# Kernel optimization log

Measured on AMD Instinct MI355X. Metric: run time of the kernel, lower is better.

Reference implementation:

```python
import jax, jax.numpy as jnp
import numpy as np

NUM_HEADS = 16
EPS = 1e-06


def setup_inputs() -> dict:
    key = jax.random.key(0)
    ks = jax.random.split(key, 6)
    b, s, d = 4, 4096, 1024
    scale = 1.0 / np.sqrt(d)
    return {
        "x": jax.random.normal(ks[0], (b, s, d), dtype=jnp.float32),
        "wq": jax.random.normal(ks[1], (d, d), dtype=jnp.float32) * scale,
        "wk": jax.random.normal(ks[2], (d, d), dtype=jnp.float32) * scale,
        "wv": jax.random.normal(ks[3], (d, d), dtype=jnp.float32) * scale,
        "wo": jax.random.normal(ks[4], (d, d), dtype=jnp.float32) * scale,
        "bo": jnp.zeros((d,), dtype=jnp.float32),
    }


def _split_heads(t, h):
    b, s, d = t.shape
    return t.reshape(b, s, h, d // h).transpose(0, 2, 1, 3)  # [b,h,s,dh]


def reference(x, wq, wk, wv, wo, bo):
    h = NUM_HEADS
    # torch Linear: y = x @ W.T (no bias for q/k/v)
    q = _split_heads(x @ wq.T, h)
    k = _split_heads(x @ wk.T, h)
    v = _split_heads(x @ wv.T, h)
    # ELU+1 feature map
    qf = jax.nn.elu(q) + 1.0
    kf = jax.nn.elu(k) + 1.0
    # global key feature sum over sequence: [b,h,dh]
    k_sum = jnp.sum(kf, axis=-2)
    # denominator: [b,h,s,1]
    denom = jnp.sum(qf * k_sum[:, :, None, :], axis=-1, keepdims=True) + EPS
    # kv = sum_s kf_s (outer) v_s  -> [b,h,dh,dh]  (the broadcast-sum in torch == matmul)
    kv = jnp.einsum('bhsd,bhse->bhde', kf, v)
    # q_kv: [b,h,s,dh]
    q_kv = jnp.einsum('bhsd,bhde->bhse', qf, kv)
    out = q_kv / denom
    b, _, s, dh = out.shape
    out = out.transpose(0, 2, 1, 3).reshape(b, s, h * dh)  # merge heads
    return out @ wo.T + bo
```

## Files before the change

### kernel.cpp

```cpp
#include <hip/hip_runtime.h>
#include <hip/hip_bf16.h>
#include <cmath>


#define TOK    16384
#define DMODEL 1024
#define NHEAD  16
#define DH     64
#define KSPLIT 8

using bf16x8 = __attribute__((ext_vector_type(8))) short;
using f32x4  = __attribute__((ext_vector_type(4))) float;

typedef __attribute__((address_space(1))) const unsigned int gld_src_t;
typedef __attribute__((address_space(3))) unsigned int gld_dst_t;

__device__ __forceinline__ unsigned short f2bf(float x) {
    unsigned int u = __float_as_uint(x);
    u += 0x7fffu + ((u >> 16) & 1u);
    return (unsigned short)(u >> 16);
}
__device__ __forceinline__ float bf2f(unsigned short b) {
    return __uint_as_float((unsigned int)b << 16);
}

__global__ __launch_bounds__(256) void split_k(
    const float* __restrict__ in, unsigned short* __restrict__ hi,
    unsigned short* __restrict__ lo, int n)
{
    int i = (blockIdx.x * 256 + threadIdx.x) * 4;
    if (i >= n) return;
    float4 v = *(const float4*)(in + i);
    float vs[4] = {v.x, v.y, v.z, v.w};
    unsigned short hh[4], ll[4];
#pragma unroll
    for (int j = 0; j < 4; ++j) {
        unsigned short h = f2bf(vs[j]);
        hh[j] = h;
        ll[j] = f2bf(vs[j] - bf2f(h));
    }
    *(ushort4*)(hi + i) = make_ushort4(hh[0], hh[1], hh[2], hh[3]);
    *(ushort4*)(lo + i) = make_ushort4(ll[0], ll[1], ll[2], ll[3]);
}

__global__ __launch_bounds__(256) void splitw_k(
    const float* __restrict__ w0, const float* __restrict__ w1,
    const float* __restrict__ w2, const float* __restrict__ w3,
    unsigned short* __restrict__ hs, unsigned short* __restrict__ ls)
{
    int w = blockIdx.x >> 10;
    const float* src = (w == 0) ? w0 : (w == 1) ? w1 : (w == 2) ? w2 : w3;
    int i = ((blockIdx.x & 1023) * 256 + threadIdx.x) * 4;
    size_t base = (size_t)w * (DMODEL * DMODEL);
    float4 v = *(const float4*)(src + i);
    float vs[4] = {v.x, v.y, v.z, v.w};
    unsigned short hh[4], ll[4];
#pragma unroll
    for (int j = 0; j < 4; ++j) {
        unsigned short h = f2bf(vs[j]);
        hh[j] = h;
        ll[j] = f2bf(vs[j] - bf2f(h));
    }
    *(ushort4*)(hs + base + i) = make_ushort4(hh[0], hh[1], hh[2], hh[3]);
    *(ushort4*)(ls + base + i) = make_ushort4(ll[0], ll[1], ll[2], ll[3]);
}

template<int ACT>
__global__ __launch_bounds__(512, 2) void gemm256_k(
    const unsigned short* __restrict__ Ah, const unsigned short* __restrict__ Al,
    const unsigned short* __restrict__ Bh, const unsigned short* __restrict__ Bl,
    const float* __restrict__ bias, float* __restrict__ C,
    unsigned short* __restrict__ Ch, unsigned short* __restrict__ Cl,
    int M, int N, int K)
{
    __shared__ unsigned short lds[2][4][256 * 32];
    const int tid  = threadIdx.x;
    const int lane = tid & 63, wid = tid >> 6;

    const int nwg = gridDim.x, cpx = nwg >> 3;
    const int g = ((int)blockIdx.x & 7) * cpx + ((int)blockIdx.x >> 3);
    const int m0 = (g >> 2) * 256, n0 = (g & 3) * 256;

    const int wr = wid >> 2, wc = wid & 3;
    const int fr = lane & 15, ko = lane >> 4;

    f32x4 acc[8][4];
#pragma unroll
    for (int i = 0; i < 8; ++i)
#pragma unroll
        for (int j = 0; j < 4; ++j) acc[i][j] = (f32x4){0.f, 0.f, 0.f, 0.f};

    const unsigned short* srcb = (wid < 2) ? Ah : (wid < 4) ? Al : (wid < 6) ? Bh : Bl;
    const int rowbase = ((wid < 4) ? m0 : n0) + (wid & 1) * 128;
    const int rloc = (wid & 1) * 128 + (lane >> 2);
    const int sslot = (lane & 3) ^ ((rloc >> 1) & 3);
    const unsigned short* gsrc0 = srcb + (size_t)(rowbase + (lane >> 2)) * K + sslot * 8;
    const int mat  = wid >> 1;
    const int ldso = ((wid & 1) * 128) * 32;

    const int koff = (ko ^ ((fr >> 1) & 3)) * 8;
    const int abase = (wr * 128 + fr) * 32 + koff;
    const int bbase = (wc * 64 + fr) * 32 + koff;
    const int nt = K / 32;

#pragma unroll
    for (int u = 0; u < 8; ++u) {
        __builtin_amdgcn_global_load_lds((gld_src_t*)(gsrc0 + (size_t)u * 16 * K),
            (gld_dst_t*)&lds[0][mat][ldso + u * 512], 16, 0, 0);
    }
    asm volatile("s_waitcnt vmcnt(0)" ::: "memory");
    __builtin_amdgcn_s_barrier();

    for (int t = 0; t < nt; ++t) {
        const int cur = t & 1;
        const bool hv = (t + 1 < nt);
        const unsigned short* gk = gsrc0 + (size_t)(t + 1) * 32;
        unsigned short* ldsn = &lds[cur ^ 1][mat][ldso];
        bf16x8 Bh_[4], Bl_[4];

#pragma unroll
        for (int p = 0; p < 4; ++p) {
            if (hv) {
#pragma unroll
                for (int q = 0; q < 2; ++q) {
                    int u = p * 2 + q;
                    __builtin_amdgcn_global_load_lds((gld_src_t*)(gk + (size_t)u * 16 * K),
                        (gld_dst_t*)(ldsn + u * 512), 16, 0, 0);
                }
            }
            if (p == 0) {
                if (hv) asm volatile("s_waitcnt vmcnt(2)" ::: "memory");
                else    asm volatile("s_waitcnt vmcnt(0)" ::: "memory");
                __builtin_amdgcn_s_barrier();
            }
            int aoff0 = abase + (2 * p) * 16 * 32;
            bf16x8 ah0 = *(const bf16x8*)&lds[cur][0][aoff0];
            bf16x8 al0 = *(const bf16x8*)&lds[cur][1][aoff0];
            bf16x8 ah1 = *(const bf16x8*)&lds[cur][0][aoff0 + 512];
            bf16x8 al1 = *(const bf16x8*)&lds[cur][1][aoff0 + 512];
            if (p == 0) {
#pragma unroll
                for (int nj = 0; nj < 4; ++nj) {
                    int boff = bbase + nj * 16 * 32;
                    Bh_[nj] = *(const bf16x8*)&lds[cur][2][boff];
                    Bl_[nj] = *(const bf16x8*)&lds[cur][3][boff];
                }
            }
            __builtin_amdgcn_s_barrier();
            asm volatile("s_waitcnt lgkmcnt(0)" ::: "memory");
            __builtin_amdgcn_sched_barrier(0);
            __builtin_amdgcn_s_setprio(1);
#pragma unroll
            for (int nj = 0; nj < 4; ++nj) {
                acc[2*p  ][nj] = __builtin_amdgcn_mfma_f32_16x16x32_bf16(ah0, Bh_[nj], acc[2*p  ][nj], 0, 0, 0);
                acc[2*p  ][nj] = __builtin_amdgcn_mfma_f32_16x16x32_bf16(ah0, Bl_[nj], acc[2*p  ][nj], 0, 0, 0);
                acc[2*p  ][nj] = __builtin_amdgcn_mfma_f32_16x16x32_bf16(al0, Bh_[nj], acc[2*p  ][nj], 0, 0, 0);
                acc[2*p+1][nj] = __builtin_amdgcn_mfma_f32_16x16x32_bf16(ah1, Bh_[nj], acc[2*p+1][nj], 0, 0, 0);
                acc[2*p+1][nj] = __builtin_amdgcn_mfma_f32_16x16x32_bf16(ah1, Bl_[nj], acc[2*p+1][nj], 0, 0, 0);
                acc[2*p+1][nj] = __builtin_amdgcn_mfma_f32_16x16x32_bf16(al1, Bh_[nj], acc[2*p+1][nj], 0, 0, 0);
            }
            __builtin_amdgcn_s_setprio(0);
            __builtin_amdgcn_s_barrier();
        }
    }

    const int fq = ko;
#pragma unroll
    for (int mi = 0; mi < 8; ++mi) {
#pragma unroll
        for (int i = 0; i < 4; ++i) {
            int m = m0 + wr * 128 + mi * 16 + fq * 4 + i;
            size_t rbase = (size_t)m * N + n0 + wc * 64;
#pragma unroll
            for (int nj = 0; nj < 4; ++nj) {
                int n = nj * 16 + fr;
                float v = acc[mi][nj][i];
                if (ACT == 1 || ACT == 3) v = (v > 0.f) ? (v + 1.f) : expf(v);
                if (ACT == 2) v += bias[n0 + wc * 64 + n];
                if (ACT == 3) {
                    unsigned short hb = f2bf(v);
                    Ch[rbase + n] = hb;
                    Cl[rbase + n] = f2bf(v - bf2f(hb));
                } else {
                    C[rbase + n] = v;
                }
            }
        }
    }
}

__global__ __launch_bounds__(256) void kv_partial_k(
    const float* __restrict__ kf, const float* __restrict__ vchunk,
    int bh_base, float* __restrict__ kvp, float* __restrict__ ksp)
{
    __shared__ float kfs[8][64];
    __shared__ float vs[8][64];
    const int bh = bh_base + blockIdx.x;
    const int split = blockIdx.y;
    const int b = bh >> 4, h = bh & 15;
    const int blocal = b - (bh_base >> 4);
    const int tid = threadIdx.x;
    const int col = tid & 63, rg = tid >> 6;
    const int tx = tid & 15, ty = tid >> 4;
    const int di0 = ty * 4, dj0 = tx * 4;

    float acc[4][4] = {};
    float ks[4] = {0.f, 0.f, 0.f, 0.f};

    const int rows = 4096 / KSPLIT;
    const size_t kbase = ((size_t)b * 4096 + (size_t)split * rows) * DMODEL + h * DH;
    const size_t vbase = ((size_t)blocal * 4096 + (size_t)split * rows) * DMODEL + h * DH;

    for (int it = 0; it < rows / 8; ++it) {
        __syncthreads();
#pragma unroll
        for (int p = 0; p < 2; ++p) {
            int r = rg + p * 4;
            size_t o = (size_t)(it * 8 + r) * DMODEL + col;
            kfs[r][col] = kf[kbase + o];
            vs[r][col]  = vchunk[vbase + o];
        }
        __syncthreads();
#pragma unroll
        for (int r = 0; r < 8; ++r) {
            float a[4], bb[4];
#pragma unroll
            for (int i = 0; i < 4; ++i) a[i] = kfs[r][di0 + i];
#pragma unroll
            for (int j = 0; j < 4; ++j) bb[j] = vs[r][dj0 + j];
#pragma unroll
            for (int i = 0; i < 4; ++i)
#pragma unroll
                for (int j = 0; j < 4; ++j)
                    acc[i][j] = fmaf(a[i], bb[j], acc[i][j]);
            if (tx == 0) {
#pragma unroll
                for (int i = 0; i < 4; ++i) ks[i] += a[i];
            }
        }
    }

    const size_t obase = ((size_t)(bh * KSPLIT + split)) * (DH * DH);
#pragma unroll
    for (int i = 0; i < 4; ++i)
#pragma unroll
        for (int j = 0; j < 4; ++j)
            kvp[obase + (size_t)(di0 + i) * DH + dj0 + j] = acc[i][j];
    if (tx == 0) {
        size_t kb = ((size_t)(bh * KSPLIT + split)) * DH + di0;
#pragma unroll
        for (int i = 0; i < 4; ++i) ksp[kb + i] = ks[i];
    }
}

__global__ __launch_bounds__(256) void reduce_kv_k(
    const float* __restrict__ kvp, const float* __restrict__ ksp,
    unsigned short* __restrict__ kvth, unsigned short* __restrict__ kvtl)
{
    int idx = blockIdx.x * 256 + threadIdx.x;
    int bh = idx >> 12, off = idx & 4095;
    int d = off & 63, e = off >> 6;
    float s = 0.f;
    for (int c = 0; c < KSPLIT; ++c) s += kvp[((size_t)(bh * KSPLIT + c)) * 4096 + d * 64 + e];
    unsigned short hb = f2bf(s);
    size_t o = (size_t)bh * (96 * 64) + (size_t)e * 64 + d;
    kvth[o] = hb;
    kvtl[o] = f2bf(s - bf2f(hb));
    if (idx < 64 * DH) {
        int bh2 = idx >> 6, d2 = idx & 63;
        float t = 0.f;
        for (int c = 0; c < KSPLIT; ++c) t += ksp[((size_t)(bh2 * KSPLIT + c)) * DH + d2];
        unsigned short h2 = f2bf(t);
        size_t o2 = (size_t)bh2 * (96 * 64) + 64 * 64 + d2;
        kvth[o2] = h2;
        kvtl[o2] = f2bf(t - bf2f(h2));
    }
}

__global__ __launch_bounds__(512, 2) void attn_mfma_k(
    const unsigned short* __restrict__ qh, const unsigned short* __restrict__ ql,
    const unsigned short* __restrict__ kvth, const unsigned short* __restrict__ kvtl,
    unsigned short* __restrict__ out_hi, unsigned short* __restrict__ out_lo)
{
    __shared__ unsigned short lds[28672];
    __shared__ float denoms[128];
    const int tid = threadIdx.x, lane = tid & 63, wid = tid >> 6;
    const int blk = blockIdx.x;
    const int bh = blk >> 5, tb = blk & 31;
    const int b = bh >> 4, h = bh & 15;
    const int t0 = b * 4096 + tb * 128;

    const int l8 = lane >> 3, s7 = lane & 7;
#pragma unroll
    for (int shot = 0; shot < 7; ++shot) {
        int r = wid * 7 + shot;
        const unsigned short* src;
        int dstE;
        if (r < 32) {
            int row = (r & 15) * 8 + l8;
            int sslot = s7 ^ (row & 7);
            src = ((r < 16) ? qh : ql) + (size_t)(t0 + row) * DMODEL + h * DH + sslot * 8;
            dstE = ((r < 16) ? 0 : 8192) + (r & 15) * 512;
        } else {
            int rb = r - 32;
            int rl = (rb < 12) ? rb : rb - 12;
            int row = rl * 8 + l8;
            int sslot = s7 ^ (row & 7);
            src = ((rb < 12) ? kvth : kvtl) + (size_t)bh * (96 * 64) + row * 64 + sslot * 8;
            dstE = ((rb < 12) ? 16384 : 22528) + rl * 512;
        }
        __builtin_amdgcn_global_load_lds((gld_src_t*)src, (gld_dst_t*)&lds[dstE], 16, 0, 0);
    }
    __syncthreads();

    const int fr = lane & 15, ko = lane >> 4, fq = ko;
    const int arow = wid * 16 + fr;

    f32x4 acc[5];
#pragma unroll
    for (int nj = 0; nj < 5; ++nj) acc[nj] = (f32x4){0.f, 0.f, 0.f, 0.f};

#pragma unroll
    for (int kt = 0; kt < 2; ++kt) {
        int aoff = arow * 64 + ((kt * 4 + ko) ^ (arow & 7)) * 8;
        bf16x8 a_h = *(const bf16x8*)&lds[aoff];
        bf16x8 a_l = *(const bf16x8*)&lds[8192 + aoff];
#pragma unroll
        for (int nj = 0; nj < 5; ++nj) {
            int brow = nj * 16 + fr;
            int boff = brow * 64 + ((kt * 4 + ko) ^ (brow & 7)) * 8;
            bf16x8 b_h = *(const bf16x8*)&lds[16384 + boff];
            bf16x8 b_l = *(const bf16x8*)&lds[22528 + boff];
            acc[nj] = __builtin_amdgcn_mfma_f32_16x16x32_bf16(a_h, b_h, acc[nj], 0, 0, 0);
            acc[nj] = __builtin_amdgcn_mfma_f32_16x16x32_bf16(a_h, b_l, acc[nj], 0, 0, 0);
            acc[nj] = __builtin_amdgcn_mfma_f32_16x16x32_bf16(a_l, b_h, acc[nj], 0, 0, 0);
        }
    }

    if (fr == 0) {
#pragma unroll
        for (int i = 0; i < 4; ++i)
            denoms[wid * 16 + fq * 4 + i] = acc[4][i] + 1e-6f;
    }
    __syncthreads();

#pragma unroll
    for (int i = 0; i < 4; ++i) {
        int row = wid * 16 + fq * 4 + i;
        float dinv = 1.0f / denoms[row];
        size_t rbase = (size_t)(t0 + row) * DMODEL + h * DH;
#pragma unroll
        for (int nj = 0; nj < 4; ++nj) {
            float v = acc[nj][i] * dinv;
            unsigned short hb = f2bf(v);
            out_hi[rbase + nj * 16 + fr] = hb;
            out_lo[rbase + nj * 16 + fr] = f2bf(v - bf2f(hb));
        }
    }
}

extern "C" void kernel_launch(void* const* d_in, const int* in_sizes, int n_in,
                              void* d_out, int out_size, void* d_ws, size_t ws_size,
                              hipStream_t stream)
{
    const float* x  = (const float*)d_in[0];
    const float* wq = (const float*)d_in[1];
    const float* wk = (const float*)d_in[2];
    const float* wv = (const float*)d_in[3];
    const float* wo = (const float*)d_in[4];
    const float* bo = (const float*)d_in[5];
    float* out = (float*)d_out;

    const size_t XE = (size_t)TOK * DMODEL;
    const size_t WE = (size_t)DMODEL * DMODEL;
    const size_t CE = (size_t)8192 * DMODEL;

    unsigned short* xh = (unsigned short*)d_ws;
    unsigned short* xl = xh + XE;
    unsigned short* wh = xl + XE;
    unsigned short* wl = wh + 4 * WE;
    float* kf   = (float*)(wl + 4 * WE);
    float* vc   = kf + XE;
    float* kvp  = vc + CE;
    float* ksp  = kvp + (size_t)64 * KSPLIT * DH * DH;
    unsigned short* kvth = (unsigned short*)(ksp + (size_t)64 * KSPLIT * DH);
    unsigned short* kvtl = kvth + (size_t)64 * 96 * 64;
    unsigned short* qh = (unsigned short*)kf;
    unsigned short* ql = qh + XE;

    split_k<<<(int)(XE / 1024), 256, 0, stream>>>(x, xh, xl, (int)XE);
    splitw_k<<<4096, 256, 0, stream>>>(wq, wk, wv, wo, wh, wl);

    const int gfull = (TOK / 256) * 4;
    const int ghalf = (8192 / 256) * 4;

    gemm256_k<1><<<gfull, 512, 0, stream>>>(xh, xl, wh + WE, wl + WE, nullptr, kf, nullptr, nullptr, TOK, DMODEL, DMODEL);

    gemm256_k<0><<<ghalf, 512, 0, stream>>>(xh, xl, wh + 2 * WE, wl + 2 * WE, nullptr, vc, nullptr, nullptr, 8192, DMODEL, DMODEL);
    kv_partial_k<<<dim3(32, KSPLIT), 256, 0, stream>>>(kf, vc, 0, kvp, ksp);

    gemm256_k<0><<<ghalf, 512, 0, stream>>>(xh + CE, xl + CE, wh + 2 * WE, wl + 2 * WE, nullptr, vc, nullptr, nullptr, 8192, DMODEL, DMODEL);
    kv_partial_k<<<dim3(32, KSPLIT), 256, 0, stream>>>(kf, vc, 32, kvp, ksp);

    reduce_kv_k<<<dim3(64 * DH * DH / 256), 256, 0, stream>>>(kvp, ksp, kvth, kvtl);

    gemm256_k<3><<<gfull, 512, 0, stream>>>(xh, xl, wh, wl, nullptr, nullptr, qh, ql, TOK, DMODEL, DMODEL);
    attn_mfma_k<<<2048, 512, 0, stream>>>(qh, ql, kvth, kvtl, xh, xl);

    gemm256_k<2><<<gfull, 512, 0, stream>>>(xh, xl, wh + 3 * WE, wl + 3 * WE, bo, out, nullptr, nullptr, TOK, DMODEL, DMODEL);
}
```

Before: 553.6 us.

## Cut per-k-step barriers in the double-buffered GEMM loop to two

The GEMM main loop is restructured so each k-tile iteration uses only two workgroup barriers at its start. Previously there were a barrier plus a full LDS wait before and after every MFMA sub-block. The next tile's global-to-LDS loads are issued in pairs alongside the A-fragment reads, and B fragments are loaded once per tile up front. The prologue no longer waits on its own loads; the first iteration's vmcnt wait covers them. The aim is to cut barrier stalls and let MFMA work overlap LDS reads and prefetch. The cost is that ordering now depends on the compiler inserting the LDS waits that were previously explicit.

```diff
diff --git a/kernel.cpp b/kernel.cpp
--- a/kernel.cpp
+++ b/kernel.cpp
@@ -108,47 +108,48 @@
         __builtin_amdgcn_global_load_lds((gld_src_t*)(gsrc0 + (size_t)u * 16 * K),
             (gld_dst_t*)&lds[0][mat][ldso + u * 512], 16, 0, 0);
     }
-    asm volatile("s_waitcnt vmcnt(0)" ::: "memory");
-    __builtin_amdgcn_s_barrier();
 
     for (int t = 0; t < nt; ++t) {
         const int cur = t & 1;
         const bool hv = (t + 1 < nt);
         const unsigned short* gk = gsrc0 + (size_t)(t + 1) * 32;
         unsigned short* ldsn = &lds[cur ^ 1][mat][ldso];
+
+        __builtin_amdgcn_s_barrier();
+        if (hv) {
+#pragma unroll
+            for (int u = 0; u < 2; ++u)
+                __builtin_amdgcn_global_load_lds((gld_src_t*)(gk + (size_t)u * 16 * K),
+                    (gld_dst_t*)(ldsn + u * 512), 16, 0, 0);
+            asm volatile("s_waitcnt vmcnt(2)" ::: "memory");
+        } else {
+            asm volatile("s_waitcnt vmcnt(0)" ::: "memory");
+        }
+        __builtin_amdgcn_s_barrier();
+        __builtin_amdgcn_sched_barrier(0);
+
         bf16x8 Bh_[4], Bl_[4];
+#pragma unroll
+        for (int nj = 0; nj < 4; ++nj) {
+            Bh_[nj] = *(const bf16x8*)&lds[cur][2][bbase + nj * 512];
+            Bl_[nj] = *(const bf16x8*)&lds[cur][3][bbase + nj * 512];
+        }
 
 #pragma unroll
         for (int p = 0; p < 4; ++p) {
-            if (hv) {
-#pragma unroll
-                for (int q = 0; q < 2; ++q) {
-                    int u = p * 2 + q;
-                    __builtin_amdgcn_global_load_lds((gld_src_t*)(gk + (size_t)u * 16 * K),
-                        (gld_dst_t*)(ldsn + u * 512), 16, 0, 0);
+            int off0 = abase + (2 * p) * 512;
+            bf16x8 ah0 = *(const bf16x8*)&lds[cur][0][off0];
+            bf16x8 al0 = *(const bf16x8*)&lds[cur][1][off0];
+            bf16x8 ah1 = *(const bf16x8*)&lds[cur][0][off0 + 512];
+            bf16x8 al1 = *(const bf16x8*)&lds[cur][1][off0 + 512];
+            if (hv && p < 3) {
+#pragma unroll
+                for (int u = 0; u < 2; ++u) {
+                    int s = 2 * p + 2 + u;
+                    __builtin_amdgcn_global_load_lds((gld_src_t*)(gk + (size_t)s * 16 * K),
+                        (gld_dst_t*)(ldsn + s * 512), 16, 0, 0);
                 }
             }
-            if (p == 0) {
-                if (hv) asm volatile("s_waitcnt vmcnt(2)" ::: "memory");
-                else    asm volatile("s_waitcnt vmcnt(0)" ::: "memory");
-                __builtin_amdgcn_s_barrier();
-            }
-            int aoff0 = abase + (2 * p) * 16 * 32;
-            bf16x8 ah0 = *(const bf16x8*)&lds[cur][0][aoff0];
-            bf16x8 al0 = *(const bf16x8*)&lds[cur][1][aoff0];
-            bf16x8 ah1 = *(const bf16x8*)&lds[cur][0][aoff0 + 512];
-            bf16x8 al1 = *(const bf16x8*)&lds[cur][1][aoff0 + 512];
-            if (p == 0) {
-#pragma unroll
-                for (int nj = 0; nj < 4; ++nj) {
-                    int boff = bbase + nj * 16 * 32;
-                    Bh_[nj] = *(const bf16x8*)&lds[cur][2][boff];
-                    Bl_[nj] = *(const bf16x8*)&lds[cur][3][boff];
-                }
-            }
-            __builtin_amdgcn_s_barrier();
-            asm volatile("s_waitcnt lgkmcnt(0)" ::: "memory");
-            __builtin_amdgcn_sched_barrier(0);
             __builtin_amdgcn_s_setprio(1);
 #pragma unroll
             for (int nj = 0; nj < 4; ++nj) {
@@ -160,7 +161,6 @@
                 acc[2*p+1][nj] = __builtin_amdgcn_mfma_f32_16x16x32_bf16(al1, Bh_[nj], acc[2*p+1][nj], 0, 0, 0);
             }
             __builtin_amdgcn_s_setprio(0);
-            __builtin_amdgcn_s_barrier();
         }
     }
 
```

After: 544.1 us. About the same (-1.7%).
